# Kernel tuning notes

Measured on AMD Instinct MI355X. Metric: run time of the kernel, lower is better.

## Reference

```python
import jax, jax.numpy as jnp
import numpy as np


def setup_inputs() -> dict:
    key = jax.random.key(0)
    k1, k2, k3, k4, k5 = jax.random.split(key, 5)
    b, t_q, t_k = 4, 256, 1024
    qs, ms, n = 512, 512, 128
    return {
        "query": jax.random.normal(k1, (b, t_q, qs), dtype=jnp.float32),
        "keys": jax.random.normal(k2, (b, t_k, ms), dtype=jnp.float32),
        "Wq": jax.random.normal(k3, (qs, n), dtype=jnp.float32) * 0.05,
        "Wk": jax.random.normal(k4, (ms, n), dtype=jnp.float32) * 0.05,
        "linear_att": jax.random.normal(k5, (n,), dtype=jnp.float32) * 0.05,
    }


def reference(query, keys, Wq, Wk, linear_att):
    # projections: b t_q n and b t_k n
    att_query = jnp.einsum("bqd,dn->bqn", query, Wq)
    att_keys = jnp.einsum("bkd,dn->bkn", keys, Wk)
    # Bahdanau additive score: tanh(q + k) . v  -> b t_q t_k
    sum_qk = att_query[:, :, None, :] + att_keys[:, None, :, :]
    scores = jnp.einsum("bqkn,n->bqk", jnp.tanh(sum_qk), linear_att)
    weights = jax.nn.softmax(scores, axis=-1)
    context = jnp.einsum("bqk,bkd->bqd", weights, keys)
    return (context, weights)
```

## Files before the change

### kernel.cpp

```cpp
#include <hip/hip_runtime.h>

#define B 4
#define TQ 256
#define TK 1024
#define QS 512
#define NN 128

#define TANH_SCALE 2.8853900817779268f
#define LOG2E 1.4426950408889634f

__device__ __forceinline__ float fast_exp2(float x) {
#if __has_builtin(__builtin_amdgcn_exp2f)
    return __builtin_amdgcn_exp2f(x);
#else
    return exp2f(x);
#endif
}
__device__ __forceinline__ float fast_rcp(float x) {
#if __has_builtin(__builtin_amdgcn_rcpf)
    return __builtin_amdgcn_rcpf(x);
#else
    return 1.0f / x;
#endif
}

__global__ __launch_bounds__(256) void proj_kernel(
    const float* __restrict__ query, const float* __restrict__ keys,
    const float* __restrict__ Wq, const float* __restrict__ Wk,
    float* __restrict__ attq, float* __restrict__ attkT)
{
    __shared__ float As[32][36];
    __shared__ float Bs[32][132];

    const int tid = threadIdx.x;
    const int rb = blockIdx.x * 32;
    const bool isq = (rb < B * TQ);
    const float* A = isq ? (query + (size_t)rb * QS)
                         : (keys + (size_t)(rb - B * TQ) * QS);
    const float* W = isq ? Wq : Wk;

    const int n0 = (tid & 31) * 4;
    const int q0 = (tid >> 5) * 4;
    float acc[4][4] = {};

    for (int k0 = 0; k0 < QS; k0 += 32) {
        {
            const int r = tid >> 3, c = tid & 7;
            const float4 v = *(const float4*)(A + (size_t)r * QS + k0 + c * 4);
            As[c * 4 + 0][r] = v.x;
            As[c * 4 + 1][r] = v.y;
            As[c * 4 + 2][r] = v.z;
            As[c * 4 + 3][r] = v.w;
        }
        {
            const int n = (tid & 31) * 4, r0 = tid >> 5;
            #pragma unroll
            for (int j = 0; j < 4; ++j) {
                const int kk = r0 + j * 8;
                *(float4*)&Bs[kk][n] =
                    *(const float4*)(W + (size_t)(k0 + kk) * NN + n);
            }
        }
        __syncthreads();
        #pragma unroll
        for (int kk = 0; kk < 32; ++kk) {
            const float4 a = *(const float4*)&As[kk][q0];
            const float4 b = *(const float4*)&Bs[kk][n0];
            const float av[4] = {a.x, a.y, a.z, a.w};
            const float bv[4] = {b.x, b.y, b.z, b.w};
            #pragma unroll
            for (int i = 0; i < 4; ++i)
                #pragma unroll
                for (int j = 0; j < 4; ++j)
                    acc[i][j] = fmaf(av[i], bv[j], acc[i][j]);
        }
        __syncthreads();
    }

    if (isq) {
        float* out = attq + (size_t)rb * NN;
        #pragma unroll
        for (int i = 0; i < 4; ++i) {
            float4 o;
            o.x = acc[i][0] * TANH_SCALE;
            o.y = acc[i][1] * TANH_SCALE;
            o.z = acc[i][2] * TANH_SCALE;
            o.w = acc[i][3] * TANH_SCALE;
            *(float4*)(out + (size_t)(q0 + i) * NN + n0) = o;
        }
    } else {
        #pragma unroll
        for (int i = 0; i < 4; ++i) {
            float4 o;
            o.x = acc[i][0] * TANH_SCALE;
            o.y = acc[i][1] * TANH_SCALE;
            o.z = acc[i][2] * TANH_SCALE;
            o.w = acc[i][3] * TANH_SCALE;
            *(float4*)&Bs[q0 + i][n0] = o;
        }
        __syncthreads();
        const int rk = rb - B * TQ;
        const int bb = rk >> 10;
        const int kbase = rk & 1023;
        const int n = tid >> 1;
        const int kh = (tid & 1) * 16;
        float* o = attkT + (size_t)bb * NN * TK + (size_t)n * TK + kbase + kh;
        #pragma unroll
        for (int m4 = 0; m4 < 4; ++m4) {
            float4 t;
            t.x = Bs[kh + m4 * 4 + 0][n];
            t.y = Bs[kh + m4 * 4 + 1][n];
            t.z = Bs[kh + m4 * 4 + 2][n];
            t.w = Bs[kh + m4 * 4 + 3][n];
            *(float4*)(o + m4 * 4) = t;
        }
    }
}

__global__ __launch_bounds__(256) void score_softmax_kernel(
    const float* __restrict__ attq, const float* __restrict__ attkT,
    const float* __restrict__ vatt, float* __restrict__ wout,
    float4* __restrict__ ctxz)
{
    __shared__ float aqs[2][128];
    __shared__ float vsm[128];
    __shared__ float red[2][8];

    const int tid = threadIdx.x;
    const int b = blockIdx.x >> 7;
    const int q0 = (blockIdx.x & 127) * 2;

    ctxz[(size_t)blockIdx.x * 256 + tid] = make_float4(0.f, 0.f, 0.f, 0.f);

    if (tid < 128) {
        aqs[0][tid] = attq[((size_t)b * TQ + q0) * NN + tid];
        vsm[tid] = vatt[tid];
    } else {
        aqs[1][tid & 127] = attq[((size_t)b * TQ + q0 + 1) * NN + (tid & 127)];
    }
    __syncthreads();

    const float* kt = attkT + (size_t)b * NN * TK + (size_t)tid * 4;
    float s[2][4] = {};

    #pragma unroll 4
    for (int n = 0; n < 128; ++n) {
        const float4 a = *(const float4*)(kt + (size_t)n * TK);
        const float a0 = aqs[0][n], a1 = aqs[1][n], vv = vsm[n];
        const float av[4] = {a.x, a.y, a.z, a.w};
        #pragma unroll
        for (int r = 0; r < 4; ++r) {
            const float x0 = a0 + av[r];
            const float t0 = fmaf(-2.f, fast_rcp(1.f + fast_exp2(x0)), 1.f);
            s[0][r] = fmaf(vv, t0, s[0][r]);
            const float x1 = a1 + av[r];
            const float t1 = fmaf(-2.f, fast_rcp(1.f + fast_exp2(x1)), 1.f);
            s[1][r] = fmaf(vv, t1, s[1][r]);
        }
    }

    const int lane = tid & 63, wid = tid >> 6;
    #pragma unroll
    for (int qq = 0; qq < 2; ++qq) {
        float mm = fmaxf(fmaxf(s[qq][0], s[qq][1]), fmaxf(s[qq][2], s[qq][3]));
        #pragma unroll
        for (int off = 32; off > 0; off >>= 1)
            mm = fmaxf(mm, __shfl_xor(mm, off, 64));
        if (lane == 0) red[qq][wid] = mm;
    }
    __syncthreads();
    float m[2];
    m[0] = fmaxf(fmaxf(red[0][0], red[0][1]), fmaxf(red[0][2], red[0][3]));
    m[1] = fmaxf(fmaxf(red[1][0], red[1][1]), fmaxf(red[1][2], red[1][3]));

    float e[2][4];
    #pragma unroll
    for (int qq = 0; qq < 2; ++qq) {
        float ls = 0.f;
        #pragma unroll
        for (int i = 0; i < 4; ++i) {
            e[qq][i] = fast_exp2((s[qq][i] - m[qq]) * LOG2E);
            ls += e[qq][i];
        }
        #pragma unroll
        for (int off = 32; off > 0; off >>= 1)
            ls += __shfl_xor(ls, off, 64);
        if (lane == 0) red[qq][4 + wid] = ls;
    }
    __syncthreads();
    #pragma unroll
    for (int qq = 0; qq < 2; ++qq) {
        const float S = red[qq][4] + red[qq][5] + red[qq][6] + red[qq][7];
        const float inv = fast_rcp(S);
        float4 w4;
        w4.x = e[qq][0] * inv; w4.y = e[qq][1] * inv;
        w4.z = e[qq][2] * inv; w4.w = e[qq][3] * inv;
        *(float4*)(wout + ((size_t)b * TQ + q0 + qq) * TK + (size_t)tid * 4) = w4;
    }
}

__global__ __launch_bounds__(256) void context_kernel(
    const float* __restrict__ keys, const float* __restrict__ w,
    float* __restrict__ ctx)
{
    __shared__ float Wst[32][34];
    __shared__ float Ks[32][64];

    const int tid = threadIdx.x;
    const int bid = blockIdx.x;
    const int b = bid >> 7;
    const int rem = bid & 127;
    const int qt = rem >> 4;
    const int dt = (rem >> 1) & 7;
    const int ks = rem & 1;

    const float* wb = w + (size_t)b * TQ * TK + (size_t)qt * 32 * TK + ks * 512;
    const float* kb = keys + (size_t)b * TK * QS + (size_t)ks * 512 * QS + dt * 64;

    const int d0 = (tid & 15) * 4;
    const int q0 = (tid >> 4) * 2;
    float acc[2][4] = {};

    for (int k0 = 0; k0 < 512; k0 += 32) {
        {
            const int r = tid >> 3, c = tid & 7;
            const float4 v = *(const float4*)(wb + (size_t)r * TK + k0 + c * 4);
            Wst[c * 4 + 0][r] = v.x;
            Wst[c * 4 + 1][r] = v.y;
            Wst[c * 4 + 2][r] = v.z;
            Wst[c * 4 + 3][r] = v.w;
        }
        {
            const int c = tid & 15, r = tid >> 4;
            *(float4*)&Ks[r][c * 4] =
                *(const float4*)(kb + (size_t)(k0 + r) * QS + c * 4);
            *(float4*)&Ks[r + 16][c * 4] =
                *(const float4*)(kb + (size_t)(k0 + r + 16) * QS + c * 4);
        }
        __syncthreads();
        #pragma unroll
        for (int kk = 0; kk < 32; ++kk) {
            const float2 a = *(const float2*)&Wst[kk][q0];
            const float4 bb = *(const float4*)&Ks[kk][d0];
            acc[0][0] = fmaf(a.x, bb.x, acc[0][0]);
            acc[0][1] = fmaf(a.x, bb.y, acc[0][1]);
            acc[0][2] = fmaf(a.x, bb.z, acc[0][2]);
            acc[0][3] = fmaf(a.x, bb.w, acc[0][3]);
            acc[1][0] = fmaf(a.y, bb.x, acc[1][0]);
            acc[1][1] = fmaf(a.y, bb.y, acc[1][1]);
            acc[1][2] = fmaf(a.y, bb.z, acc[1][2]);
            acc[1][3] = fmaf(a.y, bb.w, acc[1][3]);
        }
        __syncthreads();
    }

    float* op = ctx + ((size_t)b * TQ + qt * 32 + q0) * QS + dt * 64 + d0;
    #pragma unroll
    for (int i = 0; i < 2; ++i)
        #pragma unroll
        for (int j = 0; j < 4; ++j)
            atomicAdd(op + (size_t)i * QS + j, acc[i][j]);
}

extern "C" void kernel_launch(void* const* d_in, const int* in_sizes, int n_in,
                              void* d_out, int out_size, void* d_ws, size_t ws_size,
                              hipStream_t stream) {
    const float* query = (const float*)d_in[0];
    const float* keys  = (const float*)d_in[1];
    const float* Wq    = (const float*)d_in[2];
    const float* Wk    = (const float*)d_in[3];
    const float* vatt  = (const float*)d_in[4];

    float* ctx = (float*)d_out;
    float* wts = ctx + (size_t)B * TQ * QS;

    float* attq  = (float*)d_ws;
    float* attkT = attq + (size_t)B * TQ * NN;

    hipLaunchKernelGGL(proj_kernel, dim3((B * TQ + B * TK) / 32), dim3(256), 0,
                       stream, query, keys, Wq, Wk, attq, attkT);
    hipLaunchKernelGGL(score_softmax_kernel, dim3(B * TQ / 2), dim3(256), 0,
                       stream, attq, attkT, vatt, wts, (float4*)ctx);
    hipLaunchKernelGGL(context_kernel, dim3(512), dim3(256), 0,
                       stream, keys, wts, ctx);
}
```

Baseline: 163.3 us.

## Shrink projection and context tiles, drop split-K atomics and ctx zeroing

The projection kernel now gives each block 8 rows instead of 32, so it launches four times as many blocks, each thread computing 4 outputs. The context kernel drops the split-K with atomicAdd and the zeroing pass in the score kernel. Each block now covers 16 queries across the full key length and writes results with plain stores. The score loop unroll goes from 4 to 8. The smaller tiles add parallelism but lower register-level data reuse, so each thread issues more LDS and global loads per FMA.

Measured after the change: 162.7 us. No clear change (-0.3%).

```diff
diff --git a/kernel.cpp b/kernel.cpp
--- a/kernel.cpp
+++ b/kernel.cpp
@@ -8,6 +8,7 @@
 
 #define TANH_SCALE 2.8853900817779268f
 #define LOG2E 1.4426950408889634f
+#define CTX_ELEMS ((size_t)B * TQ * QS)
 
 __device__ __forceinline__ float fast_exp2(float x) {
 #if __has_builtin(__builtin_amdgcn_exp2f)
@@ -29,28 +30,24 @@
     const float* __restrict__ Wq, const float* __restrict__ Wk,
     float* __restrict__ attq, float* __restrict__ attkT)
 {
-    __shared__ float As[32][36];
+    __shared__ float As[32][9];
     __shared__ float Bs[32][132];
 
     const int tid = threadIdx.x;
-    const int rb = blockIdx.x * 32;
+    const int rb = blockIdx.x * 8;
     const bool isq = (rb < B * TQ);
     const float* A = isq ? (query + (size_t)rb * QS)
                          : (keys + (size_t)(rb - B * TQ) * QS);
     const float* W = isq ? Wq : Wk;
 
     const int n0 = (tid & 31) * 4;
-    const int q0 = (tid >> 5) * 4;
-    float acc[4][4] = {};
+    const int r  = tid >> 5;
+    float acc[4] = {};
 
     for (int k0 = 0; k0 < QS; k0 += 32) {
         {
-            const int r = tid >> 3, c = tid & 7;
-            const float4 v = *(const float4*)(A + (size_t)r * QS + k0 + c * 4);
-            As[c * 4 + 0][r] = v.x;
-            As[c * 4 + 1][r] = v.y;
-            As[c * 4 + 2][r] = v.z;
-            As[c * 4 + 3][r] = v.w;
+            const int rr = tid >> 5, c = tid & 31;
+            As[c][rr] = A[(size_t)rr * QS + k0 + c];
         }
         {
             const int n = (tid & 31) * 4, r0 = tid >> 5;
@@ -64,63 +61,48 @@
         __syncthreads();
         #pragma unroll
         for (int kk = 0; kk < 32; ++kk) {
-            const float4 a = *(const float4*)&As[kk][q0];
+            const float a = As[kk][r];
             const float4 b = *(const float4*)&Bs[kk][n0];
-            const float av[4] = {a.x, a.y, a.z, a.w};
-            const float bv[4] = {b.x, b.y, b.z, b.w};
-            #pragma unroll
-            for (int i = 0; i < 4; ++i)
-                #pragma unroll
-                for (int j = 0; j < 4; ++j)
-                    acc[i][j] = fmaf(av[i], bv[j], acc[i][j]);
+            acc[0] = fmaf(a, b.x, acc[0]);
+            acc[1] = fmaf(a, b.y, acc[1]);
+            acc[2] = fmaf(a, b.z, acc[2]);
+            acc[3] = fmaf(a, b.w, acc[3]);
         }
         __syncthreads();
     }
 
     if (isq) {
-        float* out = attq + (size_t)rb * NN;
-        #pragma unroll
-        for (int i = 0; i < 4; ++i) {
-            float4 o;
-            o.x = acc[i][0] * TANH_SCALE;
-            o.y = acc[i][1] * TANH_SCALE;
-            o.z = acc[i][2] * TANH_SCALE;
-            o.w = acc[i][3] * TANH_SCALE;
-            *(float4*)(out + (size_t)(q0 + i) * NN + n0) = o;
-        }
+        float4 o;
+        o.x = acc[0] * TANH_SCALE;
+        o.y = acc[1] * TANH_SCALE;
+        o.z = acc[2] * TANH_SCALE;
+        o.w = acc[3] * TANH_SCALE;
+        *(float4*)(attq + (size_t)(rb + r) * NN + n0) = o;
     } else {
-        #pragma unroll
-        for (int i = 0; i < 4; ++i) {
-            float4 o;
-            o.x = acc[i][0] * TANH_SCALE;
-            o.y = acc[i][1] * TANH_SCALE;
-            o.z = acc[i][2] * TANH_SCALE;
-            o.w = acc[i][3] * TANH_SCALE;
-            *(float4*)&Bs[q0 + i][n0] = o;
-        }
+        float4 o;
+        o.x = acc[0] * TANH_SCALE;
+        o.y = acc[1] * TANH_SCALE;
+        o.z = acc[2] * TANH_SCALE;
+        o.w = acc[3] * TANH_SCALE;
+        *(float4*)&Bs[r][n0] = o;
         __syncthreads();
         const int rk = rb - B * TQ;
         const int bb = rk >> 10;
         const int kbase = rk & 1023;
         const int n = tid >> 1;
-        const int kh = (tid & 1) * 16;
-        float* o = attkT + (size_t)bb * NN * TK + (size_t)n * TK + kbase + kh;
-        #pragma unroll
-        for (int m4 = 0; m4 < 4; ++m4) {
-            float4 t;
-            t.x = Bs[kh + m4 * 4 + 0][n];
-            t.y = Bs[kh + m4 * 4 + 1][n];
-            t.z = Bs[kh + m4 * 4 + 2][n];
-            t.w = Bs[kh + m4 * 4 + 3][n];
-            *(float4*)(o + m4 * 4) = t;
-        }
+        const int kh = (tid & 1) * 4;
+        float4 t;
+        t.x = Bs[kh + 0][n];
+        t.y = Bs[kh + 1][n];
+        t.z = Bs[kh + 2][n];
+        t.w = Bs[kh + 3][n];
+        *(float4*)(attkT + (size_t)bb * NN * TK + (size_t)n * TK + kbase + kh) = t;
     }
 }
 
 __global__ __launch_bounds__(256) void score_softmax_kernel(
     const float* __restrict__ attq, const float* __restrict__ attkT,
-    const float* __restrict__ vatt, float* __restrict__ wout,
-    float4* __restrict__ ctxz)
+    const float* __restrict__ vatt, float* __restrict__ wout)
 {
     __shared__ float aqs[2][128];
     __shared__ float vsm[128];
@@ -129,8 +111,6 @@
     const int tid = threadIdx.x;
     const int b = blockIdx.x >> 7;
     const int q0 = (blockIdx.x & 127) * 2;
-
-    ctxz[(size_t)blockIdx.x * 256 + tid] = make_float4(0.f, 0.f, 0.f, 0.f);
 
     if (tid < 128) {
         aqs[0][tid] = attq[((size_t)b * TQ + q0) * NN + tid];
@@ -143,19 +123,19 @@
     const float* kt = attkT + (size_t)b * NN * TK + (size_t)tid * 4;
     float s[2][4] = {};
 
-    #pragma unroll 4
+    #pragma unroll 8
     for (int n = 0; n < 128; ++n) {
         const float4 a = *(const float4*)(kt + (size_t)n * TK);
         const float a0 = aqs[0][n], a1 = aqs[1][n], vv = vsm[n];
         const float av[4] = {a.x, a.y, a.z, a.w};
         #pragma unroll
-        for (int r = 0; r < 4; ++r) {
-            const float x0 = a0 + av[r];
+        for (int rr = 0; rr < 4; ++rr) {
+            const float x0 = a0 + av[rr];
             const float t0 = fmaf(-2.f, fast_rcp(1.f + fast_exp2(x0)), 1.f);
-            s[0][r] = fmaf(vv, t0, s[0][r]);
-            const float x1 = a1 + av[r];
+            s[0][rr] = fmaf(vv, t0, s[0][rr]);
+            const float x1 = a1 + av[rr];
             const float t1 = fmaf(-2.f, fast_rcp(1.f + fast_exp2(x1)), 1.f);
-            s[1][r] = fmaf(vv, t1, s[1][r]);
+            s[1][rr] = fmaf(vv, t1, s[1][rr]);
         }
     }
 
@@ -203,63 +183,53 @@
     const float* __restrict__ keys, const float* __restrict__ w,
     float* __restrict__ ctx)
 {
-    __shared__ float Wst[32][34];
+    __shared__ float Wst[32][17];
     __shared__ float Ks[32][64];
 
     const int tid = threadIdx.x;
     const int bid = blockIdx.x;
     const int b = bid >> 7;
     const int rem = bid & 127;
-    const int qt = rem >> 4;
-    const int dt = (rem >> 1) & 7;
-    const int ks = rem & 1;
-
-    const float* wb = w + (size_t)b * TQ * TK + (size_t)qt * 32 * TK + ks * 512;
-    const float* kb = keys + (size_t)b * TK * QS + (size_t)ks * 512 * QS + dt * 64;
+    const int qt = rem >> 3;
+    const int dt = rem & 7;
+
+    const float* wb = w + (size_t)b * TQ * TK + (size_t)qt * 16 * TK;
+    const float* kb = keys + (size_t)b * TK * QS + dt * 64;
 
     const int d0 = (tid & 15) * 4;
-    const int q0 = (tid >> 4) * 2;
-    float acc[2][4] = {};
-
-    for (int k0 = 0; k0 < 512; k0 += 32) {
-        {
-            const int r = tid >> 3, c = tid & 7;
-            const float4 v = *(const float4*)(wb + (size_t)r * TK + k0 + c * 4);
-            Wst[c * 4 + 0][r] = v.x;
-            Wst[c * 4 + 1][r] = v.y;
-            Wst[c * 4 + 2][r] = v.z;
-            Wst[c * 4 + 3][r] = v.w;
-        }
-        {
-            const int c = tid & 15, r = tid >> 4;
-            *(float4*)&Ks[r][c * 4] =
-                *(const float4*)(kb + (size_t)(k0 + r) * QS + c * 4);
-            *(float4*)&Ks[r + 16][c * 4] =
-                *(const float4*)(kb + (size_t)(k0 + r + 16) * QS + c * 4);
+    const int q  = tid >> 4;
+    float acc[4] = {};
+
+    for (int k0 = 0; k0 < TK; k0 += 32) {
+        {
+            const int rr = tid >> 4, c = (tid & 15) * 2;
+            const float2 v = *(const float2*)(wb + (size_t)rr * TK + k0 + c);
+            Wst[c + 0][rr] = v.x;
+            Wst[c + 1][rr] = v.y;
+        }
+        {
+            const int c = tid & 15, rr = tid >> 4;
+            *(float4*)&Ks[rr][c * 4] =
+                *(const float4*)(kb + (size_t)(k0 + rr) * QS + c * 4);
+            *(float4*)&Ks[rr + 16][c * 4] =
+                *(const float4*)(kb + (size_t)(k0 + rr + 16) * QS + c * 4);
         }
         __syncthreads();
         #pragma unroll
         for (int kk = 0; kk < 32; ++kk) {
-            const float2 a = *(const float2*)&Wst[kk][q0];
+            const float a = Wst[kk][q];
             const float4 bb = *(const float4*)&Ks[kk][d0];
-            acc[0][0] = fmaf(a.x, bb.x, acc[0][0]);
-            acc[0][1] = fmaf(a.x, bb.y, acc[0][1]);
-            acc[0][2] = fmaf(a.x, bb.z, acc[0][2]);
-            acc[0][3] = fmaf(a.x, bb.w, acc[0][3]);
-            acc[1][0] = fmaf(a.y, bb.x, acc[1][0]);
-            acc[1][1] = fmaf(a.y, bb.y, acc[1][1]);
-            acc[1][2] = fmaf(a.y, bb.z, acc[1][2]);
-            acc[1][3] = fmaf(a.y, bb.w, acc[1][3]);
-        }
-        __syncthreads();
-    }
-
-    float* op = ctx + ((size_t)b * TQ + qt * 32 + q0) * QS + dt * 64 + d0;
-    #pragma unroll
-    for (int i = 0; i < 2; ++i)
-        #pragma unroll
-        for (int j = 0; j < 4; ++j)
-            atomicAdd(op + (size_t)i * QS + j, acc[i][j]);
+            acc[0] = fmaf(a, bb.x, acc[0]);
+            acc[1] = fmaf(a, bb.y, acc[1]);
+            acc[2] = fmaf(a, bb.z, acc[2]);
+            acc[3] = fmaf(a, bb.w, acc[3]);
+        }
+        __syncthreads();
+    }
+
+    float4 o;
+    o.x = acc[0]; o.y = acc[1]; o.z = acc[2]; o.w = acc[3];
+    *(float4*)(ctx + ((size_t)b * TQ + qt * 16 + q) * QS + dt * 64 + d0) = o;
 }
 
 extern "C" void kernel_launch(void* const* d_in, const int* in_sizes, int n_in,
@@ -272,15 +242,15 @@
     const float* vatt  = (const float*)d_in[4];
 
     float* ctx = (float*)d_out;
-    float* wts = ctx + (size_t)B * TQ * QS;
+    float* wts = ctx + CTX_ELEMS;
 
     float* attq  = (float*)d_ws;
     float* attkT = attq + (size_t)B * TQ * NN;
 
-    hipLaunchKernelGGL(proj_kernel, dim3((B * TQ + B * TK) / 32), dim3(256), 0,
+    hipLaunchKernelGGL(proj_kernel, dim3((B * TQ + B * TK) / 8), dim3(256), 0,
                        stream, query, keys, Wq, Wk, attq, attkT);
     hipLaunchKernelGGL(score_softmax_kernel, dim3(B * TQ / 2), dim3(256), 0,
-                       stream, attq, attkT, vatt, wts, (float4*)ctx);
+                       stream, attq, attkT, vatt, wts);
     hipLaunchKernelGGL(context_kernel, dim3(512), dim3(256), 0,
                        stream, keys, wts, ctx);
 }
```
